# Kernel tuning notes

Hardware: AMD Instinct MI355X
Metric: run time of the kernel (lower is better)

Reference implementation:

```python
import jax, jax.numpy as jnp
import numpy as np

B, V, H = 128, 50257, 2048   # batch, vocab, history length
NEG_INF = jnp.float32(-jnp.inf)
TEMP_MIN = 1e-5


def setup_inputs() -> dict:
    key = jax.random.key(0)
    k1, k2, k3 = jax.random.split(key, 3)
    logits = jax.random.normal(k1, (B, V), jnp.float32) * 4.0
    previous_tokens = jax.random.randint(k2, (B, H), 0, V)
    # uniform noise for the exponential-race (Gumbel-max) draw; strictly positive
    u = jax.random.uniform(k3, (B, V), jnp.float32, minval=1e-10, maxval=1.0)
    return {
        "logits": logits,
        "previous_tokens": previous_tokens,
        "u": u,
        "top_p": jnp.full((1,), 0.9, jnp.float32),
        "repetition_penalty": jnp.full((1,), 1.35, jnp.float32),
        "temperature": jnp.full((1,), 0.7, jnp.float32),
        "top_k": 50,
    }


def _logits_to_probs(logits, previous_tokens, temperature, top_k, top_p, repetition_penalty):
    b = jnp.arange(logits.shape[0])[:, None]  # [B,1] row index for scatters
    # repetition penalty: gather history scores, shrink, scatter back
    score = jnp.take_along_axis(logits, previous_tokens, axis=1)          # [B,H]
    score = jnp.where(score < 0, score * repetition_penalty, score / repetition_penalty)
    logits = logits.at[b, previous_tokens].set(score)                     # [B,V]
    # nucleus (top-p) filtering via descending sort + cumulative softmax
    order = jnp.argsort(-logits, axis=-1)                                 # [B,V]
    sorted_logits = jnp.take_along_axis(logits, order, axis=1)
    cum_probs = jnp.cumsum(jax.nn.softmax(sorted_logits, axis=-1), axis=-1)
    remove_sorted = cum_probs > top_p
    remove_sorted = remove_sorted.at[:, 0].set(False)                     # keep best token
    # scatter removal mask back to vocab order (order is a permutation)
    remove = jnp.zeros_like(remove_sorted).at[b, order].set(remove_sorted)
    logits = jnp.where(remove, NEG_INF, logits)
    # temperature + top-k pivot filter
    logits = logits / jnp.maximum(temperature, TEMP_MIN)
    v = jax.lax.top_k(logits, top_k)[0]                                   # [B,top_k]
    pivot = v[:, -1:]
    logits = jnp.where(logits < pivot, NEG_INF, logits)
    return jax.nn.softmax(logits, axis=-1)


def reference(logits, previous_tokens, u, top_p, repetition_penalty, temperature, top_k):
    previous_tokens = previous_tokens.astype(jnp.int32)
    probs = _logits_to_probs(logits, previous_tokens, temperature, top_k, top_p,
                             repetition_penalty)
    # multinomial_sample_one_no_sync: exponential race argmax(probs / Exp(1))
    q = -jnp.log(u)
    idx_next = jnp.argmax(probs / q, axis=-1, keepdims=True).astype(jnp.int32)
    return idx_next, probs
```

## Files before the change

### kernel.cpp

```cpp
#include <hip/hip_runtime.h>
#include <cfloat>
#include <cmath>
#include <cstdint>

#define VV 50257
#define SPLITS 4
#define CHUNKA 12568
#define BMW ((CHUNKA + 31) / 32)
#define NBUCK 4096
#define CAPC 512
#define K1T 512
#define K2T 256
#define NW1 (K1T / 64)

__device__ __forceinline__ unsigned fmono(float f) {
    unsigned b = __float_as_uint(f);
    return b ^ (((int)b < 0) ? 0xFFFFFFFFu : 0x80000000u);
}
__device__ __forceinline__ float unmono(unsigned m) {
    unsigned b = (m & 0x80000000u) ? (m ^ 0x80000000u) : ~m;
    return __uint_as_float(b);
}
__device__ __forceinline__ uint64_t mkkey(unsigned mono, int idx) {
    return ((uint64_t)mono << 32) | (unsigned)(~idx);
}

__global__ __launch_bounds__(K1T, 4) void pp_k1(
    const float* __restrict__ logits, const int* __restrict__ prev,
    const float* __restrict__ rpp,
    float* __restrict__ pm, float* __restrict__ ps,
    uint64_t* __restrict__ gkey, float* __restrict__ out_probs, int Hp)
{
    const int sp = blockIdx.x, row = blockIdx.y;
    const int tid = threadIdx.x, lane = tid & 63, wid = tid >> 6;
    const int c0 = sp * CHUNKA;
    const int c1 = min(VV, c0 + CHUNKA);
    const int len = c1 - c0;
    const float rp = rpp[0], inv_rp = 1.0f / rp;

    __shared__ unsigned bm[BMW];
    __shared__ unsigned hist[NBUCK];
    __shared__ float red_m[NW1], red_s[NW1];
    __shared__ unsigned wtot[NW1];
    __shared__ uint64_t cand_k[CAPC];
    __shared__ uint64_t top64[64];
    __shared__ float sM;
    __shared__ int sT, sCnt;

    for (int i = tid; i < BMW; i += K1T) bm[i] = 0u;
    for (int i = tid; i < NBUCK; i += K1T) hist[i] = 0u;
    if (tid == 0) { sT = 0; sCnt = 0; }
    __syncthreads();

    const int* prow = prev + (size_t)row * Hp;
    const int h4 = Hp >> 2;
    const int4* prow4 = (const int4*)prow;
    for (int i = tid; i < h4; i += K1T) {
        int4 t4 = prow4[i];
        int t;
        t = t4.x; if (t >= c0 && t < c1) { int o = t - c0; atomicOr(&bm[o >> 5], 1u << (o & 31)); }
        t = t4.y; if (t >= c0 && t < c1) { int o = t - c0; atomicOr(&bm[o >> 5], 1u << (o & 31)); }
        t = t4.z; if (t >= c0 && t < c1) { int o = t - c0; atomicOr(&bm[o >> 5], 1u << (o & 31)); }
        t = t4.w; if (t >= c0 && t < c1) { int o = t - c0; atomicOr(&bm[o >> 5], 1u << (o & 31)); }
    }
    for (int i = 4 * h4 + tid; i < Hp; i += K1T) {
        int t = prow[i];
        if (t >= c0 && t < c1) { int o = t - c0; atomicOr(&bm[o >> 5], 1u << (o & 31)); }
    }
    __syncthreads();

    const float* lrow = logits + (size_t)row * VV;
    float* orow = out_probs + (size_t)row * VV;
    const int pad = (4 - (row & 3)) & 3;
    const int n4 = (len - pad) >> 2;
    const int tail0 = pad + 4 * n4;
    const float4* l4 = (const float4*)(lrow + c0 + pad);
    float4* o4 = (float4*)(orow + c0 + pad);

    float m = -FLT_MAX;
    for (int o = tid; o < pad; o += K1T) {
        float l = lrow[c0 + o];
        if ((bm[o >> 5] >> (o & 31)) & 1u) l = (l < 0.f) ? l * rp : l * inv_rp;
        atomicAdd(&hist[fmono(l) >> 20], 1u);
        m = fmaxf(m, l);
    }
    #pragma unroll 4
    for (int k = tid; k < n4; k += K1T) {
        float4 v = l4[k];
        const int ob = pad + 4 * k;
        float x;
        x = v.x; if ((bm[(ob+0) >> 5] >> ((ob+0) & 31)) & 1u) x = (x < 0.f) ? x * rp : x * inv_rp;
        atomicAdd(&hist[fmono(x) >> 20], 1u); m = fmaxf(m, x);
        x = v.y; if ((bm[(ob+1) >> 5] >> ((ob+1) & 31)) & 1u) x = (x < 0.f) ? x * rp : x * inv_rp;
        atomicAdd(&hist[fmono(x) >> 20], 1u); m = fmaxf(m, x);
        x = v.z; if ((bm[(ob+2) >> 5] >> ((ob+2) & 31)) & 1u) x = (x < 0.f) ? x * rp : x * inv_rp;
        atomicAdd(&hist[fmono(x) >> 20], 1u); m = fmaxf(m, x);
        x = v.w; if ((bm[(ob+3) >> 5] >> ((ob+3) & 31)) & 1u) x = (x < 0.f) ? x * rp : x * inv_rp;
        atomicAdd(&hist[fmono(x) >> 20], 1u); m = fmaxf(m, x);
    }
    for (int o = tail0 + tid; o < len; o += K1T) {
        float l = lrow[c0 + o];
        if ((bm[o >> 5] >> (o & 31)) & 1u) l = (l < 0.f) ? l * rp : l * inv_rp;
        atomicAdd(&hist[fmono(l) >> 20], 1u);
        m = fmaxf(m, l);
    }

    #pragma unroll
    for (int off = 32; off; off >>= 1) m = fmaxf(m, __shfl_down(m, off));
    if (lane == 0) red_m[wid] = m;
    __syncthreads();
    if (tid == 0) {
        float M = red_m[0];
        for (int w = 1; w < NW1; ++w) M = fmaxf(M, red_m[w]);
        sM = M;
    }

    unsigned c = 0;
    #pragma unroll
    for (int j = 0; j < 8; ++j) c += hist[tid * 8 + j];
    unsigned v = c;
    #pragma unroll
    for (int off = 1; off < 64; off <<= 1) {
        unsigned o = __shfl_down(v, off);
        if (lane + off < 64) v += o;
    }
    if (lane == 0) wtot[wid] = v;
    __syncthreads();
    unsigned add = 0;
    for (int w = wid + 1; w < NW1; ++w) add += wtot[w];
    const unsigned mySuf = v + add;
    const unsigned sufExcl = mySuf - c;
    if (mySuf >= 64u && sufExcl < 64u) {
        unsigned above = sufExcl;
        for (int b = tid * 8 + 7; b >= tid * 8; --b) {
            above += hist[b];
            if (above >= 64u) { sT = b; break; }
        }
    }
    __syncthreads();
    const unsigned T = (unsigned)sT;
    const float M = sM;

    float s = 0.0f;
    for (int o = tid; o < pad; o += K1T) {
        float l = lrow[c0 + o];
        if ((bm[o >> 5] >> (o & 31)) & 1u) l = (l < 0.f) ? l * rp : l * inv_rp;
        s += __expf(l - M);
        unsigned mo = fmono(l);
        if ((mo >> 20) >= T) {
            int p = atomicAdd(&sCnt, 1);
            if (p < CAPC) cand_k[p] = mkkey(mo, c0 + o);
        }
    }
    #pragma unroll 4
    for (int k = tid; k < n4; k += K1T) {
        float4 vv = l4[k];
        const int gi = c0 + pad + 4 * k;
        const int ob = pad + 4 * k;
        float x; unsigned mo;
        x = vv.x; if ((bm[(ob+0) >> 5] >> ((ob+0) & 31)) & 1u) x = (x < 0.f) ? x * rp : x * inv_rp;
        s += __expf(x - M); mo = fmono(x);
        if ((mo >> 20) >= T) { int p = atomicAdd(&sCnt, 1); if (p < CAPC) cand_k[p] = mkkey(mo, gi + 0); }
        x = vv.y; if ((bm[(ob+1) >> 5] >> ((ob+1) & 31)) & 1u) x = (x < 0.f) ? x * rp : x * inv_rp;
        s += __expf(x - M); mo = fmono(x);
        if ((mo >> 20) >= T) { int p = atomicAdd(&sCnt, 1); if (p < CAPC) cand_k[p] = mkkey(mo, gi + 1); }
        x = vv.z; if ((bm[(ob+2) >> 5] >> ((ob+2) & 31)) & 1u) x = (x < 0.f) ? x * rp : x * inv_rp;
        s += __expf(x - M); mo = fmono(x);
        if ((mo >> 20) >= T) { int p = atomicAdd(&sCnt, 1); if (p < CAPC) cand_k[p] = mkkey(mo, gi + 2); }
        x = vv.w; if ((bm[(ob+3) >> 5] >> ((ob+3) & 31)) & 1u) x = (x < 0.f) ? x * rp : x * inv_rp;
        s += __expf(x - M); mo = fmono(x);
        if ((mo >> 20) >= T) { int p = atomicAdd(&sCnt, 1); if (p < CAPC) cand_k[p] = mkkey(mo, gi + 3); }
    }
    for (int o = tail0 + tid; o < len; o += K1T) {
        float l = lrow[c0 + o];
        if ((bm[o >> 5] >> (o & 31)) & 1u) l = (l < 0.f) ? l * rp : l * inv_rp;
        s += __expf(l - M);
        unsigned mo = fmono(l);
        if ((mo >> 20) >= T) {
            int p = atomicAdd(&sCnt, 1);
            if (p < CAPC) cand_k[p] = mkkey(mo, c0 + o);
        }
    }
    #pragma unroll
    for (int off = 32; off; off >>= 1) s += __shfl_down(s, off);
    if (lane == 0) red_s[wid] = s;
    __syncthreads();

    const int slot = row * SPLITS + sp;
    if (tid == 0) {
        float Ss = red_s[0];
        for (int w = 1; w < NW1; ++w) Ss += red_s[w];
        pm[slot] = M;
        ps[slot] = Ss;
    }

    const int cnt = min(sCnt, CAPC);
    for (int t = tid; t < cnt; t += K1T) {
        const uint64_t ki = cand_k[t];
        int r = 0;
        int j = 0;
        for (; j + 8 <= cnt; j += 8) {
            uint64_t a0 = cand_k[j],   a1 = cand_k[j+1], a2 = cand_k[j+2], a3 = cand_k[j+3];
            uint64_t a4 = cand_k[j+4], a5 = cand_k[j+5], a6 = cand_k[j+6], a7 = cand_k[j+7];
            r += (int)(a0 > ki) + (int)(a1 > ki) + (int)(a2 > ki) + (int)(a3 > ki)
               + (int)(a4 > ki) + (int)(a5 > ki) + (int)(a6 > ki) + (int)(a7 > ki);
        }
        for (; j < cnt; ++j) r += (int)(cand_k[j] > ki);
        if (r < 64) top64[r] = ki;
    }
    __syncthreads();
    if (tid < 64) gkey[(size_t)slot * 64 + tid] = top64[tid];

    for (int o = tid; o < pad; o += K1T) orow[c0 + o] = 0.f;
    const float4 z4 = make_float4(0.f, 0.f, 0.f, 0.f);
    for (int k = tid; k < n4; k += K1T) o4[k] = z4;
    for (int o = tail0 + tid; o < len; o += K1T) orow[c0 + o] = 0.f;
}

__global__ __launch_bounds__(K2T) void pp_k2(
    const float* __restrict__ u, const float* __restrict__ toppp,
    const float* __restrict__ tempp, const int* __restrict__ topkp,
    const float* __restrict__ pm, const float* __restrict__ ps,
    const uint64_t* __restrict__ gkey,
    float* __restrict__ out_idx, float* __restrict__ out_probs)
{
    const int row = blockIdx.x, tid = threadIdx.x;
    __shared__ uint64_t ck[SPLITS * 64];
    __shared__ uint64_t tk[64];
    __shared__ float sM, sS;

    ck[tid] = gkey[(size_t)row * (SPLITS * 64) + tid];
    if (tid == 0) {
        float M = pm[row * SPLITS], S = ps[row * SPLITS];
        for (int j = 1; j < SPLITS; ++j) {
            float m2 = pm[row * SPLITS + j], s2 = ps[row * SPLITS + j];
            float nm = fmaxf(M, m2);
            S = S * __expf(M - nm) + s2 * __expf(m2 - nm);
            M = nm;
        }
        sM = M; sS = S;
    }
    __syncthreads();

    {
        const int j = tid >> 6;
        const uint64_t ki = ck[tid];
        int r = tid & 63;
        #pragma unroll
        for (int o = 0; o < SPLITS; ++o) {
            if (o == j) continue;
            const uint64_t* ls = &ck[o * 64];
            int lo = 0, hi = 64;
            while (lo < hi) {
                int mid = (lo + hi) >> 1;
                if (ls[mid] > ki) lo = mid + 1; else hi = mid;
            }
            r += lo;
        }
        if (r < 64) tk[r] = ki;
    }
    __syncthreads();

    if (tid < 64) {
        const int lane = tid;
        const float top_p = toppp[0];
        const float temp = tempp[0];
        int K = topkp[0]; K = min(max(K, 1), 64);
        const float M = sM, Ssum = sS;
        const uint64_t k64 = tk[lane];
        const float vl = unmono((unsigned)(k64 >> 32));
        const int ci = (int)(~(unsigned)(k64 & 0xFFFFFFFFu));
        bool act = (lane < K);
        float e = act ? expf(vl - M) / Ssum : 0.0f;
        float cum = e;
        #pragma unroll
        for (int off2 = 1; off2 < 64; off2 <<= 1) {
            float pv = __shfl_up(cum, off2);
            if (lane >= off2) cum += pv;
        }
        unsigned long long bal = __ballot(act && (cum <= top_p));
        int n = (int)__popcll(bal);
        if (n < 1) n = 1;
        const float v0 = __shfl(vl, 0);
        const float invT = 1.0f / fmaxf(temp, 1e-5f);
        bool keep = (lane < n);
        float w = keep ? expf((vl - v0) * invT) : 0.0f;
        float Z = w;
        #pragma unroll
        for (int off2 = 32; off2; off2 >>= 1) Z += __shfl_xor(Z, off2);
        float p = keep ? (w / Z) : 0.0f;
        if (keep) out_probs[(size_t)row * VV + ci] = p;
        float ratio = -1.0f;
        if (keep) ratio = p / (-logf(u[(size_t)row * VV + ci]));
        int bi = keep ? ci : 0x7FFFFFFF;
        #pragma unroll
        for (int off2 = 32; off2; off2 >>= 1) {
            float orat = __shfl_xor(ratio, off2);
            int oidx = __shfl_xor(bi, off2);
            if (orat > ratio || (orat == ratio && oidx < bi)) { ratio = orat; bi = oidx; }
        }
        if (lane == 0) out_idx[row] = (float)bi;
    }
}

extern "C" void kernel_launch(void* const* d_in, const int* in_sizes, int n_in,
                              void* d_out, int out_size, void* d_ws, size_t ws_size,
                              hipStream_t stream) {
    const float* logits = (const float*)d_in[0];
    const int*   prev   = (const int*)d_in[1];
    const float* u      = (const float*)d_in[2];
    const float* topp   = (const float*)d_in[3];
    const float* rp     = (const float*)d_in[4];
    const float* temp   = (const float*)d_in[5];
    const int*   topk   = (const int*)d_in[6];

    const int B  = in_sizes[0] / VV;
    const int Hp = in_sizes[1] / B;

    char* ws = (char*)d_ws;
    float* pm = (float*)ws;
    float* ps = pm + (size_t)B * SPLITS;
    uint64_t* gkey = (uint64_t*)(ws + 16384);

    float* out = (float*)d_out;
    pp_k1<<<dim3(SPLITS, B), K1T, 0, stream>>>(
        logits, prev, rp, pm, ps, gkey, out + B, Hp);
    pp_k2<<<B, K2T, 0, stream>>>(
        u, topp, temp, topk, pm, ps, gkey, out, out + B);
}
```

Measured before the change: 29.39 us.

## Fuse online softmax sum into first pass and double vocab splits per row

The first pass now keeps an online max/sum-exp, merged across lanes and warps with rescaling, so the second pass only gathers candidates. Zeroing of the output probs moves into the first pass as well. Each row is split 8 ways instead of 4, and the candidate capacity, merge-kernel thread count and unroll factors are adjusted to match. This trades two branchy exp evaluations per element and more merge work for more blocks in flight and one less reduction phase. The halved candidate buffer could overflow if many values tie in the threshold bucket.

```diff
diff --git a/kernel.cpp b/kernel.cpp
--- a/kernel.cpp
+++ b/kernel.cpp
@@ -4,13 +4,13 @@
 #include <cstdint>
 
 #define VV 50257
-#define SPLITS 4
-#define CHUNKA 12568
+#define SPLITS 8
+#define CHUNKA 6284
 #define BMW ((CHUNKA + 31) / 32)
 #define NBUCK 4096
-#define CAPC 512
+#define CAPC 256
 #define K1T 512
-#define K2T 256
+#define K2T 512
 #define NW1 (K1T / 64)
 
 __device__ __forceinline__ unsigned fmono(float f) {
@@ -25,7 +25,7 @@
     return ((uint64_t)mono << 32) | (unsigned)(~idx);
 }
 
-__global__ __launch_bounds__(K1T, 4) void pp_k1(
+__global__ __launch_bounds__(K1T) void pp_k1(
     const float* __restrict__ logits, const int* __restrict__ prev,
     const float* __restrict__ rpp,
     float* __restrict__ pm, float* __restrict__ ps,
@@ -44,7 +44,6 @@
     __shared__ unsigned wtot[NW1];
     __shared__ uint64_t cand_k[CAPC];
     __shared__ uint64_t top64[64];
-    __shared__ float sM;
     __shared__ int sT, sCnt;
 
     for (int i = tid; i < BMW; i += K1T) bm[i] = 0u;
@@ -76,43 +75,65 @@
     const int tail0 = pad + 4 * n4;
     const float4* l4 = (const float4*)(lrow + c0 + pad);
     float4* o4 = (float4*)(orow + c0 + pad);
-
-    float m = -FLT_MAX;
+    const float4 z4 = make_float4(0.f, 0.f, 0.f, 0.f);
+
+    float m = -FLT_MAX, s = 0.0f;
     for (int o = tid; o < pad; o += K1T) {
         float l = lrow[c0 + o];
+        orow[c0 + o] = 0.f;
         if ((bm[o >> 5] >> (o & 31)) & 1u) l = (l < 0.f) ? l * rp : l * inv_rp;
         atomicAdd(&hist[fmono(l) >> 20], 1u);
-        m = fmaxf(m, l);
-    }
-    #pragma unroll 4
+        if (l <= m) s += __expf(l - m);
+        else { s = s * __expf(m - l) + 1.0f; m = l; }
+    }
+    #pragma unroll 2
     for (int k = tid; k < n4; k += K1T) {
         float4 v = l4[k];
+        o4[k] = z4;
         const int ob = pad + 4 * k;
         float x;
         x = v.x; if ((bm[(ob+0) >> 5] >> ((ob+0) & 31)) & 1u) x = (x < 0.f) ? x * rp : x * inv_rp;
-        atomicAdd(&hist[fmono(x) >> 20], 1u); m = fmaxf(m, x);
+        atomicAdd(&hist[fmono(x) >> 20], 1u);
+        if (x <= m) s += __expf(x - m); else { s = s * __expf(m - x) + 1.0f; m = x; }
         x = v.y; if ((bm[(ob+1) >> 5] >> ((ob+1) & 31)) & 1u) x = (x < 0.f) ? x * rp : x * inv_rp;
-        atomicAdd(&hist[fmono(x) >> 20], 1u); m = fmaxf(m, x);
+        atomicAdd(&hist[fmono(x) >> 20], 1u);
+        if (x <= m) s += __expf(x - m); else { s = s * __expf(m - x) + 1.0f; m = x; }
         x = v.z; if ((bm[(ob+2) >> 5] >> ((ob+2) & 31)) & 1u) x = (x < 0.f) ? x * rp : x * inv_rp;
-        atomicAdd(&hist[fmono(x) >> 20], 1u); m = fmaxf(m, x);
+        atomicAdd(&hist[fmono(x) >> 20], 1u);
+        if (x <= m) s += __expf(x - m); else { s = s * __expf(m - x) + 1.0f; m = x; }
         x = v.w; if ((bm[(ob+3) >> 5] >> ((ob+3) & 31)) & 1u) x = (x < 0.f) ? x * rp : x * inv_rp;
-        atomicAdd(&hist[fmono(x) >> 20], 1u); m = fmaxf(m, x);
+        atomicAdd(&hist[fmono(x) >> 20], 1u);
+        if (x <= m) s += __expf(x - m); else { s = s * __expf(m - x) + 1.0f; m = x; }
     }
     for (int o = tail0 + tid; o < len; o += K1T) {
         float l = lrow[c0 + o];
+        orow[c0 + o] = 0.f;
         if ((bm[o >> 5] >> (o & 31)) & 1u) l = (l < 0.f) ? l * rp : l * inv_rp;
         atomicAdd(&hist[fmono(l) >> 20], 1u);
-        m = fmaxf(m, l);
+        if (l <= m) s += __expf(l - m);
+        else { s = s * __expf(m - l) + 1.0f; m = l; }
     }
 
     #pragma unroll
-    for (int off = 32; off; off >>= 1) m = fmaxf(m, __shfl_down(m, off));
-    if (lane == 0) red_m[wid] = m;
-    __syncthreads();
+    for (int off = 32; off; off >>= 1) {
+        float om = __shfl_down(m, off);
+        float os = __shfl_down(s, off);
+        float nm = fmaxf(m, om);
+        s = s * __expf(m - nm) + os * __expf(om - nm);
+        m = nm;
+    }
+    if (lane == 0) { red_m[wid] = m; red_s[wid] = s; }
+    __syncthreads();
+    const int slot = row * SPLITS + sp;
     if (tid == 0) {
-        float M = red_m[0];
-        for (int w = 1; w < NW1; ++w) M = fmaxf(M, red_m[w]);
-        sM = M;
+        float M = red_m[0], Ss = red_s[0];
+        for (int w = 1; w < NW1; ++w) {
+            float nm = fmaxf(M, red_m[w]);
+            Ss = Ss * __expf(M - nm) + red_s[w] * __expf(red_m[w] - nm);
+            M = nm;
+        }
+        pm[slot] = M;
+        ps[slot] = Ss;
     }
 
     unsigned c = 0;
@@ -139,60 +160,45 @@
     }
     __syncthreads();
     const unsigned T = (unsigned)sT;
-    const float M = sM;
-
-    float s = 0.0f;
+
     for (int o = tid; o < pad; o += K1T) {
         float l = lrow[c0 + o];
         if ((bm[o >> 5] >> (o & 31)) & 1u) l = (l < 0.f) ? l * rp : l * inv_rp;
-        s += __expf(l - M);
         unsigned mo = fmono(l);
         if ((mo >> 20) >= T) {
             int p = atomicAdd(&sCnt, 1);
             if (p < CAPC) cand_k[p] = mkkey(mo, c0 + o);
         }
     }
-    #pragma unroll 4
+    #pragma unroll 2
     for (int k = tid; k < n4; k += K1T) {
         float4 vv = l4[k];
         const int gi = c0 + pad + 4 * k;
         const int ob = pad + 4 * k;
         float x; unsigned mo;
         x = vv.x; if ((bm[(ob+0) >> 5] >> ((ob+0) & 31)) & 1u) x = (x < 0.f) ? x * rp : x * inv_rp;
-        s += __expf(x - M); mo = fmono(x);
+        mo = fmono(x);
         if ((mo >> 20) >= T) { int p = atomicAdd(&sCnt, 1); if (p < CAPC) cand_k[p] = mkkey(mo, gi + 0); }
         x = vv.y; if ((bm[(ob+1) >> 5] >> ((ob+1) & 31)) & 1u) x = (x < 0.f) ? x * rp : x * inv_rp;
-        s += __expf(x - M); mo = fmono(x);
+        mo = fmono(x);
         if ((mo >> 20) >= T) { int p = atomicAdd(&sCnt, 1); if (p < CAPC) cand_k[p] = mkkey(mo, gi + 1); }
         x = vv.z; if ((bm[(ob+2) >> 5] >> ((ob+2) & 31)) & 1u) x = (x < 0.f) ? x * rp : x * inv_rp;
-        s += __expf(x - M); mo = fmono(x);
+        mo = fmono(x);
         if ((mo >> 20) >= T) { int p = atomicAdd(&sCnt, 1); if (p < CAPC) cand_k[p] = mkkey(mo, gi + 2); }
         x = vv.w; if ((bm[(ob+3) >> 5] >> ((ob+3) & 31)) & 1u) x = (x < 0.f) ? x * rp : x * inv_rp;
-        s += __expf(x - M); mo = fmono(x);
+        mo = fmono(x);
         if ((mo >> 20) >= T) { int p = atomicAdd(&sCnt, 1); if (p < CAPC) cand_k[p] = mkkey(mo, gi + 3); }
     }
     for (int o = tail0 + tid; o < len; o += K1T) {
         float l = lrow[c0 + o];
         if ((bm[o >> 5] >> (o & 31)) & 1u) l = (l < 0.f) ? l * rp : l * inv_rp;
-        s += __expf(l - M);
         unsigned mo = fmono(l);
         if ((mo >> 20) >= T) {
             int p = atomicAdd(&sCnt, 1);
             if (p < CAPC) cand_k[p] = mkkey(mo, c0 + o);
         }
     }
-    #pragma unroll
-    for (int off = 32; off; off >>= 1) s += __shfl_down(s, off);
-    if (lane == 0) red_s[wid] = s;
-    __syncthreads();
-
-    const int slot = row * SPLITS + sp;
-    if (tid == 0) {
-        float Ss = red_s[0];
-        for (int w = 1; w < NW1; ++w) Ss += red_s[w];
-        pm[slot] = M;
-        ps[slot] = Ss;
-    }
+    __syncthreads();
 
     const int cnt = min(sCnt, CAPC);
     for (int t = tid; t < cnt; t += K1T) {
@@ -210,11 +216,6 @@
     }
     __syncthreads();
     if (tid < 64) gkey[(size_t)slot * 64 + tid] = top64[tid];
-
-    for (int o = tid; o < pad; o += K1T) orow[c0 + o] = 0.f;
-    const float4 z4 = make_float4(0.f, 0.f, 0.f, 0.f);
-    for (int k = tid; k < n4; k += K1T) o4[k] = z4;
-    for (int o = tail0 + tid; o < len; o += K1T) orow[c0 + o] = 0.f;
 }
 
 __global__ __launch_bounds__(K2T) void pp_k2(
```

Measured after the change: 31.59 us. +7.5%, slower.

## Replace histogram threshold with max-relative cutoff and adaptive fallback, double splits

Applied to the files above, without the earlier changes.

Drops the shared-memory 4096-bucket histogram, its atomics and the suffix scan used to find the top-64 threshold. Candidates are instead taken as logits at or above M-7, with a bisection fallback that rescans the chunk if the count falls outside [64, CAPC]. The row is also split into 8 chunks instead of 4, and the zero-fill of the output becomes nontemporal stores issued in the first pass. The cost is possible extra rescans when the fixed offset misses, and a larger second kernel block that sees more candidate keys.

```diff
diff --git a/kernel.cpp b/kernel.cpp
--- a/kernel.cpp
+++ b/kernel.cpp
@@ -4,14 +4,15 @@
 #include <cstdint>
 
 #define VV 50257
-#define SPLITS 4
-#define CHUNKA 12568
+#define SPLITS 8
+#define CHUNKA 6284
 #define BMW ((CHUNKA + 31) / 32)
-#define NBUCK 4096
-#define CAPC 512
+#define CAPC 1024
 #define K1T 512
-#define K2T 256
+#define K2T 512
 #define NW1 (K1T / 64)
+
+typedef float vf4 __attribute__((ext_vector_type(4)));
 
 __device__ __forceinline__ unsigned fmono(float f) {
     unsigned b = __float_as_uint(f);
@@ -25,7 +26,7 @@
     return ((uint64_t)mono << 32) | (unsigned)(~idx);
 }
 
-__global__ __launch_bounds__(K1T, 4) void pp_k1(
+__global__ __launch_bounds__(K1T) void pp_k1(
     const float* __restrict__ logits, const int* __restrict__ prev,
     const float* __restrict__ rpp,
     float* __restrict__ pm, float* __restrict__ ps,
@@ -39,17 +40,14 @@
     const float rp = rpp[0], inv_rp = 1.0f / rp;
 
     __shared__ unsigned bm[BMW];
-    __shared__ unsigned hist[NBUCK];
     __shared__ float red_m[NW1], red_s[NW1];
-    __shared__ unsigned wtot[NW1];
     __shared__ uint64_t cand_k[CAPC];
     __shared__ uint64_t top64[64];
-    __shared__ float sM;
-    __shared__ int sT, sCnt;
+    __shared__ int sCnt, sCnt2;
 
     for (int i = tid; i < BMW; i += K1T) bm[i] = 0u;
-    for (int i = tid; i < NBUCK; i += K1T) hist[i] = 0u;
-    if (tid == 0) { sT = 0; sCnt = 0; }
+    if (tid == 0) sCnt = 0;
+    if (tid < 64) top64[tid] = 0ull;
     __syncthreads();
 
     const int* prow = prev + (size_t)row * Hp;
@@ -75,33 +73,36 @@
     const int n4 = (len - pad) >> 2;
     const int tail0 = pad + 4 * n4;
     const float4* l4 = (const float4*)(lrow + c0 + pad);
-    float4* o4 = (float4*)(orow + c0 + pad);
+    float* obase = orow + c0;
+    vf4* o4 = (vf4*)(orow + c0 + pad);
+    const vf4 z4 = (vf4)0.0f;
 
     float m = -FLT_MAX;
     for (int o = tid; o < pad; o += K1T) {
         float l = lrow[c0 + o];
+        __builtin_nontemporal_store(0.0f, obase + o);
         if ((bm[o >> 5] >> (o & 31)) & 1u) l = (l < 0.f) ? l * rp : l * inv_rp;
-        atomicAdd(&hist[fmono(l) >> 20], 1u);
         m = fmaxf(m, l);
     }
     #pragma unroll 4
     for (int k = tid; k < n4; k += K1T) {
         float4 v = l4[k];
+        __builtin_nontemporal_store(z4, o4 + k);
         const int ob = pad + 4 * k;
         float x;
         x = v.x; if ((bm[(ob+0) >> 5] >> ((ob+0) & 31)) & 1u) x = (x < 0.f) ? x * rp : x * inv_rp;
-        atomicAdd(&hist[fmono(x) >> 20], 1u); m = fmaxf(m, x);
+        m = fmaxf(m, x);
         x = v.y; if ((bm[(ob+1) >> 5] >> ((ob+1) & 31)) & 1u) x = (x < 0.f) ? x * rp : x * inv_rp;
-        atomicAdd(&hist[fmono(x) >> 20], 1u); m = fmaxf(m, x);
+        m = fmaxf(m, x);
         x = v.z; if ((bm[(ob+2) >> 5] >> ((ob+2) & 31)) & 1u) x = (x < 0.f) ? x * rp : x * inv_rp;
-        atomicAdd(&hist[fmono(x) >> 20], 1u); m = fmaxf(m, x);
+        m = fmaxf(m, x);
         x = v.w; if ((bm[(ob+3) >> 5] >> ((ob+3) & 31)) & 1u) x = (x < 0.f) ? x * rp : x * inv_rp;
-        atomicAdd(&hist[fmono(x) >> 20], 1u); m = fmaxf(m, x);
+        m = fmaxf(m, x);
     }
     for (int o = tail0 + tid; o < len; o += K1T) {
         float l = lrow[c0 + o];
+        __builtin_nontemporal_store(0.0f, obase + o);
         if ((bm[o >> 5] >> (o & 31)) & 1u) l = (l < 0.f) ? l * rp : l * inv_rp;
-        atomicAdd(&hist[fmono(l) >> 20], 1u);
         m = fmaxf(m, l);
     }
 
@@ -109,76 +110,47 @@
     for (int off = 32; off; off >>= 1) m = fmaxf(m, __shfl_down(m, off));
     if (lane == 0) red_m[wid] = m;
     __syncthreads();
-    if (tid == 0) {
-        float M = red_m[0];
-        for (int w = 1; w < NW1; ++w) M = fmaxf(M, red_m[w]);
-        sM = M;
-    }
-
-    unsigned c = 0;
+    float M = red_m[0];
     #pragma unroll
-    for (int j = 0; j < 8; ++j) c += hist[tid * 8 + j];
-    unsigned v = c;
-    #pragma unroll
-    for (int off = 1; off < 64; off <<= 1) {
-        unsigned o = __shfl_down(v, off);
-        if (lane + off < 64) v += o;
-    }
-    if (lane == 0) wtot[wid] = v;
-    __syncthreads();
-    unsigned add = 0;
-    for (int w = wid + 1; w < NW1; ++w) add += wtot[w];
-    const unsigned mySuf = v + add;
-    const unsigned sufExcl = mySuf - c;
-    if (mySuf >= 64u && sufExcl < 64u) {
-        unsigned above = sufExcl;
-        for (int b = tid * 8 + 7; b >= tid * 8; --b) {
-            above += hist[b];
-            if (above >= 64u) { sT = b; break; }
-        }
-    }
-    __syncthreads();
-    const unsigned T = (unsigned)sT;
-    const float M = sM;
+    for (int w = 1; w < NW1; ++w) M = fmaxf(M, red_m[w]);
+    const float Tv = M - 7.0f;
 
     float s = 0.0f;
     for (int o = tid; o < pad; o += K1T) {
-        float l = lrow[c0 + o];
-        if ((bm[o >> 5] >> (o & 31)) & 1u) l = (l < 0.f) ? l * rp : l * inv_rp;
-        s += __expf(l - M);
-        unsigned mo = fmono(l);
-        if ((mo >> 20) >= T) {
+        float x = lrow[c0 + o];
+        if ((bm[o >> 5] >> (o & 31)) & 1u) x = (x < 0.f) ? x * rp : x * inv_rp;
+        s += __expf(x - M);
+        if (x >= Tv) {
             int p = atomicAdd(&sCnt, 1);
-            if (p < CAPC) cand_k[p] = mkkey(mo, c0 + o);
-        }
-    }
-    #pragma unroll 4
+            if (p < CAPC) cand_k[p] = mkkey(fmono(x), c0 + o);
+        }
+    }
+    #pragma unroll 2
     for (int k = tid; k < n4; k += K1T) {
-        float4 vv = l4[k];
-        const int gi = c0 + pad + 4 * k;
+        float4 v = l4[k];
         const int ob = pad + 4 * k;
-        float x; unsigned mo;
-        x = vv.x; if ((bm[(ob+0) >> 5] >> ((ob+0) & 31)) & 1u) x = (x < 0.f) ? x * rp : x * inv_rp;
-        s += __expf(x - M); mo = fmono(x);
-        if ((mo >> 20) >= T) { int p = atomicAdd(&sCnt, 1); if (p < CAPC) cand_k[p] = mkkey(mo, gi + 0); }
-        x = vv.y; if ((bm[(ob+1) >> 5] >> ((ob+1) & 31)) & 1u) x = (x < 0.f) ? x * rp : x * inv_rp;
-        s += __expf(x - M); mo = fmono(x);
-        if ((mo >> 20) >= T) { int p = atomicAdd(&sCnt, 1); if (p < CAPC) cand_k[p] = mkkey(mo, gi + 1); }
-        x = vv.z; if ((bm[(ob+2) >> 5] >> ((ob+2) & 31)) & 1u) x = (x < 0.f) ? x * rp : x * inv_rp;
-        s += __expf(x - M); mo = fmono(x);
-        if ((mo >> 20) >= T) { int p = atomicAdd(&sCnt, 1); if (p < CAPC) cand_k[p] = mkkey(mo, gi + 2); }
-        x = vv.w; if ((bm[(ob+3) >> 5] >> ((ob+3) & 31)) & 1u) x = (x < 0.f) ? x * rp : x * inv_rp;
-        s += __expf(x - M); mo = fmono(x);
-        if ((mo >> 20) >= T) { int p = atomicAdd(&sCnt, 1); if (p < CAPC) cand_k[p] = mkkey(mo, gi + 3); }
+        const int gi = c0 + ob;
+        float x;
+        x = v.x; if ((bm[(ob+0) >> 5] >> ((ob+0) & 31)) & 1u) x = (x < 0.f) ? x * rp : x * inv_rp;
+        s += __expf(x - M);
+        if (x >= Tv) { int p = atomicAdd(&sCnt, 1); if (p < CAPC) cand_k[p] = mkkey(fmono(x), gi + 0); }
+        x = v.y; if ((bm[(ob+1) >> 5] >> ((ob+1) & 31)) & 1u) x = (x < 0.f) ? x * rp : x * inv_rp;
+        s += __expf(x - M);
+        if (x >= Tv) { int p = atomicAdd(&sCnt, 1); if (p < CAPC) cand_k[p] = mkkey(fmono(x), gi + 1); }
+        x = v.z; if ((bm[(ob+2) >> 5] >> ((ob+2) & 31)) & 1u) x = (x < 0.f) ? x * rp : x * inv_rp;
+        s += __expf(x - M);
+        if (x >= Tv) { int p = atomicAdd(&sCnt, 1); if (p < CAPC) cand_k[p] = mkkey(fmono(x), gi + 2); }
+        x = v.w; if ((bm[(ob+3) >> 5] >> ((ob+3) & 31)) & 1u) x = (x < 0.f) ? x * rp : x * inv_rp;
+        s += __expf(x - M);
+        if (x >= Tv) { int p = atomicAdd(&sCnt, 1); if (p < CAPC) cand_k[p] = mkkey(fmono(x), gi + 3); }
     }
     for (int o = tail0 + tid; o < len; o += K1T) {
-        float l = lrow[c0 + o];
-        if ((bm[o >> 5] >> (o & 31)) & 1u) l = (l < 0.f) ? l * rp : l * inv_rp;
-        s += __expf(l - M);
-        unsigned mo = fmono(l);
-        if ((mo >> 20) >= T) {
+        float x = lrow[c0 + o];
+        if ((bm[o >> 5] >> (o & 31)) & 1u) x = (x < 0.f) ? x * rp : x * inv_rp;
+        s += __expf(x - M);
+        if (x >= Tv) {
             int p = atomicAdd(&sCnt, 1);
-            if (p < CAPC) cand_k[p] = mkkey(mo, c0 + o);
+            if (p < CAPC) cand_k[p] = mkkey(fmono(x), c0 + o);
         }
     }
     #pragma unroll
@@ -193,8 +165,41 @@
         pm[slot] = M;
         ps[slot] = Ss;
     }
-
-    const int cnt = min(sCnt, CAPC);
+    int cnt = sCnt;
+
+    if (cnt < 64 || cnt > CAPC) {
+        float tlo = -FLT_MAX, thi = M, tv = Tv;
+        for (int it = 0; it < 10 && (cnt < 64 || cnt > CAPC); ++it) {
+            if (cnt < 64) { thi = tv; tv = (tlo == -FLT_MAX) ? (M - 2.0f * (M - tv) - 8.0f) : 0.5f * (tv + tlo); }
+            else          { tlo = tv; tv = 0.5f * (tv + thi); }
+            if (tid == 0) sCnt2 = 0;
+            __syncthreads();
+            int lc = 0;
+            for (int o = tid; o < len; o += K1T) {
+                float x = lrow[c0 + o];
+                if ((bm[o >> 5] >> (o & 31)) & 1u) x = (x < 0.f) ? x * rp : x * inv_rp;
+                lc += (int)(x >= tv);
+            }
+            #pragma unroll
+            for (int off = 32; off; off >>= 1) lc += __shfl_down(lc, off);
+            if (lane == 0) atomicAdd(&sCnt2, lc);
+            __syncthreads();
+            cnt = sCnt2;
+        }
+        if (tid == 0) sCnt = 0;
+        __syncthreads();
+        for (int o = tid; o < len; o += K1T) {
+            float x = lrow[c0 + o];
+            if ((bm[o >> 5] >> (o & 31)) & 1u) x = (x < 0.f) ? x * rp : x * inv_rp;
+            if (x >= tv) {
+                int p = atomicAdd(&sCnt, 1);
+                if (p < CAPC) cand_k[p] = mkkey(fmono(x), c0 + o);
+            }
+        }
+        __syncthreads();
+        cnt = min(sCnt, CAPC);
+    }
+
     for (int t = tid; t < cnt; t += K1T) {
         const uint64_t ki = cand_k[t];
         int r = 0;
@@ -210,11 +215,6 @@
     }
     __syncthreads();
     if (tid < 64) gkey[(size_t)slot * 64 + tid] = top64[tid];
-
-    for (int o = tid; o < pad; o += K1T) orow[c0 + o] = 0.f;
-    const float4 z4 = make_float4(0.f, 0.f, 0.f, 0.f);
-    for (int k = tid; k < n4; k += K1T) o4[k] = z4;
-    for (int o = tail0 + tid; o < len; o += K1T) orow[c0 + o] = 0.f;
 }
 
 __global__ __launch_bounds__(K2T) void pp_k2(
```

New measurement: 61.22 us. +108.3%, slower.
